# Optimization experiments

Hardware: AMD Instinct MI355X
Metric: run time of the kernel (lower is better)

Reference implementation:

```python
import jax, jax.numpy as jnp
import numpy as np

B, N, M, D_MODEL, D_K, D_V = 8, 2048, 2048, 1024, 1024, 1024
NEG = -1000000000.0


def setup_inputs() -> dict:
    key = jax.random.key(0)
    ks = jax.random.split(key, 10)
    s = 1.0 / np.sqrt(D_MODEL)
    return {
        "querys": jax.random.normal(ks[0], (B, N, D_MODEL), jnp.float32),
        "keys": jax.random.normal(ks[1], (B, M, D_MODEL), jnp.float32),
        "values": jax.random.normal(ks[2], (B, M, D_MODEL), jnp.float32),
        "mask": jax.random.randint(ks[3], (N, M), 0, 2, jnp.int32),
        "Wq": jax.random.normal(ks[4], (D_K, D_MODEL), jnp.float32) * s,
        "bq": jnp.zeros((D_K,), jnp.float32),
        "Wk": jax.random.normal(ks[5], (D_K, D_MODEL), jnp.float32) * s,
        "bk": jnp.zeros((D_K,), jnp.float32),
        "Wv": jax.random.normal(ks[6], (D_V, D_MODEL), jnp.float32) * s,
        "bv": jnp.zeros((D_V,), jnp.float32),
    }


def reference(querys, keys, values, mask, Wq, bq, Wk, bk, Wv, bv):
    # Linear projections (torch Linear: x @ W.T + b)
    q = querys @ Wq.T + bq          # [B, N, Dk]
    k = keys @ Wk.T + bk            # [B, M, Dk]
    v = values @ Wv.T + bv          # [B, M, Dv]
    # Original computes QK^T via broadcast mul+sum; GEMM form is identical math.
    # NOTE: no 1/sqrt(d) scaling, matching the source.
    scores = jnp.einsum('bnd,bmd->bnm', q, k)  # [B, N, M]
    scores = jnp.where(mask[None, :, :] == 0, NEG, scores)
    weights = jax.nn.softmax(scores, axis=2)
    out = jnp.einsum('bnm,bmd->bnd', weights, v)  # [B, N, Dv]
    return out
```

## Files before the change

kernel.cpp:

```cpp
#include <hip/hip_runtime.h>
#include <cstdint>

typedef __bf16 bf16_t;
typedef __bf16 bf16x8 __attribute__((ext_vector_type(8)));
typedef float f32x4 __attribute__((ext_vector_type(4)));

#define AS1 __attribute__((address_space(1)))
#define AS3 __attribute__((address_space(3)))

__device__ __forceinline__ void gload_lds16(const bf16_t* g, bf16_t* l) {
    __builtin_amdgcn_global_load_lds((const AS1 void*)g, (AS3 void*)l, 16, 0, 0);
}
__device__ __forceinline__ f32x4 mfma_bf16(bf16x8 a, bf16x8 b, f32x4 c) {
    return __builtin_amdgcn_mfma_f32_16x16x32_bf16(a, b, c, 0, 0, 0);
}

template <bool SPLIT, int BIAS, int OUTMODE>
__global__ __launch_bounds__(256) void gemm_bt(
    const bf16_t* __restrict__ Ah, const bf16_t* __restrict__ Al, long long strideA, int lda,
    const bf16_t* __restrict__ Bh, const bf16_t* __restrict__ Bl, long long strideB, int ldb,
    void* __restrict__ C0, void* __restrict__ C1, long long strideC, int ldc,
    const float* __restrict__ bias, int K)
{
    __shared__ bf16_t Ash[128 * 32];
    __shared__ bf16_t Bsh[128 * 32];
    __shared__ bf16_t Asl[SPLIT ? 128 * 32 : 8];
    __shared__ bf16_t Bsl[SPLIT ? 128 * 32 : 8];

    const int bz = blockIdx.z;
    const int rowBase = blockIdx.y * 128;
    const int colBase = blockIdx.x * 128;
    const bf16_t* AhB = Ah + (long long)bz * strideA;
    const bf16_t* BhB = Bh + (long long)bz * strideB;
    const bf16_t* AlB = SPLIT ? Al + (long long)bz * strideA : nullptr;
    const bf16_t* BlB = SPLIT ? Bl + (long long)bz * strideB : nullptr;

    const int t = threadIdx.x;
    const int lane = t & 63;
    const int w = t >> 6;
    const int wr = (w >> 1) * 64;
    const int wc = (w & 1) * 64;

    f32x4 acc[4][4] = {};

    const int r0 = t >> 2;
    const int kc0 = (((t & 3) ^ ((r0 >> 1) & 3)) * 8);

    for (int k0 = 0; k0 < K; k0 += 32) {
        const long long aoff0 = (long long)(rowBase + r0) * lda + k0 + kc0;
        const long long aoff1 = (long long)(rowBase + r0 + 64) * lda + k0 + kc0;
        const long long boff0 = (long long)(colBase + r0) * ldb + k0 + kc0;
        const long long boff1 = (long long)(colBase + r0 + 64) * ldb + k0 + kc0;
        gload_lds16(AhB + aoff0, &Ash[t * 8]);
        gload_lds16(AhB + aoff1, &Ash[(t + 256) * 8]);
        gload_lds16(BhB + boff0, &Bsh[t * 8]);
        gload_lds16(BhB + boff1, &Bsh[(t + 256) * 8]);
        if (SPLIT) {
            gload_lds16(AlB + aoff0, &Asl[t * 8]);
            gload_lds16(AlB + aoff1, &Asl[(t + 256) * 8]);
            gload_lds16(BlB + boff0, &Bsl[t * 8]);
            gload_lds16(BlB + boff1, &Bsl[(t + 256) * 8]);
        }
        __syncthreads();

        const int fr = lane & 15;
        const int kqs = (((lane >> 4) ^ ((lane >> 1) & 3)) * 8);
        bf16x8 ah[4], bh[4], al[4], bl[4];
#pragma unroll
        for (int mi = 0; mi < 4; mi++) {
            ah[mi] = *(const bf16x8*)&Ash[(wr + mi * 16 + fr) * 32 + kqs];
            if (SPLIT) al[mi] = *(const bf16x8*)&Asl[(wr + mi * 16 + fr) * 32 + kqs];
        }
#pragma unroll
        for (int ni = 0; ni < 4; ni++) {
            bh[ni] = *(const bf16x8*)&Bsh[(wc + ni * 16 + fr) * 32 + kqs];
            if (SPLIT) bl[ni] = *(const bf16x8*)&Bsl[(wc + ni * 16 + fr) * 32 + kqs];
        }

#pragma unroll
        for (int mi = 0; mi < 4; mi++)
#pragma unroll
            for (int ni = 0; ni < 4; ni++) {
                if (SPLIT) {
                    acc[mi][ni] = mfma_bf16(al[mi], bh[ni], acc[mi][ni]);
                    acc[mi][ni] = mfma_bf16(ah[mi], bl[ni], acc[mi][ni]);
                }
                acc[mi][ni] = mfma_bf16(ah[mi], bh[ni], acc[mi][ni]);
            }
        __syncthreads();
    }

    const int fc = lane & 15;
    const int fr4 = (lane >> 4) * 4;
#pragma unroll
    for (int mi = 0; mi < 4; mi++)
#pragma unroll
        for (int ni = 0; ni < 4; ni++)
#pragma unroll
            for (int rg = 0; rg < 4; rg++) {
                const int row = rowBase + wr + mi * 16 + fr4 + rg;
                const int col = colBase + wc + ni * 16 + fc;
                float v = acc[mi][ni][rg];
                if (BIAS == 1) v += bias[col];
                else if (BIAS == 2) v += bias[row];
                const long long off = (long long)bz * strideC + (long long)row * ldc + col;
                if (OUTMODE == 0) {
                    ((float*)C0)[off] = v;
                } else if (OUTMODE == 1) {
                    ((bf16_t*)C0)[off] = (bf16_t)v;
                } else {
                    const bf16_t h = (bf16_t)v;
                    ((bf16_t*)C0)[off] = h;
                    ((bf16_t*)C1)[off] = (bf16_t)(v - (float)h);
                }
            }
}

__global__ __launch_bounds__(256) void split_f32(const float* __restrict__ x,
                                                 bf16_t* __restrict__ h,
                                                 bf16_t* __restrict__ l)
{
    const long long i = ((long long)blockIdx.x * 256 + threadIdx.x) * 4;
    const float4 v = *(const float4*)&x[i];
    bf16_t hh[4], ll[4];
    const float vv[4] = {v.x, v.y, v.z, v.w};
#pragma unroll
    for (int j = 0; j < 4; j++) {
        hh[j] = (bf16_t)vv[j];
        ll[j] = (bf16_t)(vv[j] - (float)hh[j]);
    }
    *(short4*)&h[i] = *(short4*)hh;
    *(short4*)&l[i] = *(short4*)ll;
}

__global__ __launch_bounds__(256) void cast_f32(const float* __restrict__ x,
                                                bf16_t* __restrict__ y)
{
    const long long i = ((long long)blockIdx.x * 256 + threadIdx.x) * 4;
    const float4 v = *(const float4*)&x[i];
    bf16_t hh[4] = {(bf16_t)v.x, (bf16_t)v.y, (bf16_t)v.z, (bf16_t)v.w};
    *(short4*)&y[i] = *(short4*)hh;
}

__global__ __launch_bounds__(256) void softmax_rows(const float* __restrict__ S,
                                                    bf16_t* __restrict__ P,
                                                    const int* __restrict__ mask,
                                                    int n0)
{
    __shared__ float red[4];
    const long long r = blockIdx.x;
    const float* row = S + r * 2048;
    const int* mrow = mask + (long long)(n0 + (int)(r & 2047)) * 2048;
    const int t = threadIdx.x;

    float v[8];
#pragma unroll
    for (int i = 0; i < 8; i++) {
        const int j = i * 256 + t;
        v[i] = (mrow[j] != 0) ? row[j] : -1000000000.0f;
    }
    float m = v[0];
#pragma unroll
    for (int i = 1; i < 8; i++) m = fmaxf(m, v[i]);
#pragma unroll
    for (int off = 32; off; off >>= 1) m = fmaxf(m, __shfl_xor(m, off));
    if ((t & 63) == 0) red[t >> 6] = m;
    __syncthreads();
    const float rowmax = fmaxf(fmaxf(red[0], red[1]), fmaxf(red[2], red[3]));
    __syncthreads();

    float sum = 0.0f;
    float e[8];
#pragma unroll
    for (int i = 0; i < 8; i++) { e[i] = __expf(v[i] - rowmax); sum += e[i]; }
#pragma unroll
    for (int off = 32; off; off >>= 1) sum += __shfl_xor(sum, off);
    if ((t & 63) == 0) red[t >> 6] = sum;
    __syncthreads();
    const float inv = 1.0f / (red[0] + red[1] + red[2] + red[3]);

    bf16_t* prow = P + r * 2048;
#pragma unroll
    for (int i = 0; i < 8; i++) prow[i * 256 + t] = (bf16_t)(e[i] * inv);
}

extern "C" void kernel_launch(void* const* d_in, const int* in_sizes, int n_in,
                              void* d_out, int out_size, void* d_ws, size_t ws_size,
                              hipStream_t stream) {
    constexpr int Bb = 8, N = 2048, M = 2048, D = 1024;
    constexpr long long MB = 1LL << 20;

    const float* querys = (const float*)d_in[0];
    const float* keys   = (const float*)d_in[1];
    const float* values = (const float*)d_in[2];
    const int*   mask   = (const int*)d_in[3];
    const float* Wq = (const float*)d_in[4];
    const float* bq = (const float*)d_in[5];
    const float* Wk = (const float*)d_in[6];
    const float* bk = (const float*)d_in[7];
    const float* Wv = (const float*)d_in[8];
    const float* bv = (const float*)d_in[9];
    float* out = (float*)d_out;

    const long long w = (long long)ws_size;
    auto needB = [&](long long cb) { return 10 * MB + cb * 52 * MB; };
    int CB = 0;
    if      (w >= needB(8)) CB = 8;
    else if (w >= needB(4)) CB = 4;
    else if (w >= needB(2)) CB = 2;
    else if (w >= needB(1)) CB = 1;
    const bool batched = (CB != 0);
    int NCH = N;
    if (!batched) {
        CB = 1;
        NCH = (w >= 38 * MB + 512 * 2048 * 6) ? 512 : 128;
    }

    char* ws = (char*)d_ws;
    long long o = 0;
    auto carve = [&](long long bytes) { char* p = ws + o; o += bytes; return p; };
    bf16_t* WqH = (bf16_t*)carve(2 * MB);
    bf16_t* WqL = (bf16_t*)carve(2 * MB);
    bf16_t* WkH = (bf16_t*)carve(2 * MB);
    bf16_t* WkL = (bf16_t*)carve(2 * MB);
    bf16_t* WvB = (bf16_t*)carve(2 * MB);
    bf16_t* XH  = (bf16_t*)carve((long long)CB * 4 * MB);
    bf16_t* XL  = (bf16_t*)carve((long long)CB * 4 * MB);
    bf16_t* QH  = (bf16_t*)carve((long long)CB * 4 * MB);
    bf16_t* QL  = (bf16_t*)carve((long long)CB * 4 * MB);
    bf16_t* KH  = (bf16_t*)carve((long long)CB * 4 * MB);
    bf16_t* KL  = (bf16_t*)carve((long long)CB * 4 * MB);
    bf16_t* VT  = (bf16_t*)carve((long long)CB * 4 * MB);
    float*  S   = (float*)carve(batched ? (long long)CB * N * M * 4 : (long long)NCH * 2048 * 4);
    bf16_t* P   = (bf16_t*)carve(batched ? (long long)CB * N * M * 2 : (long long)NCH * 2048 * 2);

    dim3 blk(256);
    const long long grpElems = (long long)CB * N * D;

    split_f32<<<dim3((D * D) / 1024), blk, 0, stream>>>(Wq, WqH, WqL);
    split_f32<<<dim3((D * D) / 1024), blk, 0, stream>>>(Wk, WkH, WkL);
    cast_f32<<<dim3((D * D) / 1024), blk, 0, stream>>>(Wv, WvB);

    for (int b0 = 0; b0 < Bb; b0 += CB) {
        const long long xoff = (long long)b0 * N * D;
        split_f32<<<dim3(grpElems / 1024), blk, 0, stream>>>(querys + xoff, XH, XL);
        gemm_bt<true, 1, 2><<<dim3(D / 128, CB * N / 128, 1), blk, 0, stream>>>(
            XH, XL, 0, D, WqH, WqL, 0, D, QH, QL, 0, D, bq, D);
        split_f32<<<dim3(grpElems / 1024), blk, 0, stream>>>(keys + xoff, XH, XL);
        gemm_bt<true, 1, 2><<<dim3(D / 128, CB * M / 128, 1), blk, 0, stream>>>(
            XH, XL, 0, D, WkH, WkL, 0, D, KH, KL, 0, D, bk, D);
        cast_f32<<<dim3(grpElems / 1024), blk, 0, stream>>>(values + xoff, XH);
        gemm_bt<false, 2, 1><<<dim3(M / 128, D / 128, CB), blk, 0, stream>>>(
            WvB, nullptr, 0, D, XH, nullptr, (long long)M * D, D,
            VT, nullptr, (long long)D * M, M, bv, D);

        if (batched) {
            gemm_bt<true, 0, 0><<<dim3(M / 128, N / 128, CB), blk, 0, stream>>>(
                QH, QL, (long long)N * D, D,
                KH, KL, (long long)M * D, D,
                S, nullptr, (long long)N * M, M, nullptr, D);
            softmax_rows<<<dim3(CB * N), blk, 0, stream>>>(S, P, mask, 0);
            gemm_bt<false, 0, 0><<<dim3(D / 128, N / 128, CB), blk, 0, stream>>>(
                P, nullptr, (long long)N * M, M,
                VT, nullptr, (long long)D * M, M,
                out + xoff, nullptr, (long long)N * D, D, nullptr, M);
        } else {
            for (int z = 0; z < CB; z++) {
                for (int n0 = 0; n0 < N; n0 += NCH) {
                    gemm_bt<true, 0, 0><<<dim3(M / 128, NCH / 128, 1), blk, 0, stream>>>(
                        QH + ((long long)z * N + n0) * D, QL + ((long long)z * N + n0) * D, 0, D,
                        KH + (long long)z * M * D, KL + (long long)z * M * D, 0, D,
                        S, nullptr, 0, M, nullptr, D);
                    softmax_rows<<<dim3(NCH), blk, 0, stream>>>(S, P, mask, n0);
                    gemm_bt<false, 0, 0><<<dim3(D / 128, NCH / 128, 1), blk, 0, stream>>>(
                        P, nullptr, 0, M, VT + (long long)z * D * M, nullptr, 0, M,
                        out + ((long long)(b0 + z) * N + n0) * D, nullptr, 0, D, nullptr, M);
                }
            }
        }
    }
    (void)in_sizes; (void)n_in; (void)out_size;
}
```

Measured before the change: 962.8 us.

## Replace 128x128 GEMM with 256x256 four-stage pipelined 512-thread kernel

Replaces the 128x128-tile, 256-thread GEMM with a 256x256-tile, 8-wave kernel that uses a 4-deep LDS ring buffer fed by direct global-to-LDS loads. The split-bf16 terms are flattened into a single stream of K-stages, and each stage is split into two MFMA halves interleaved with prefetches, using explicit vmcnt waits, barriers and s_setprio. This aims to hide global memory latency and raise data reuse per block. In exchange it needs 128 KB of LDS per block and more registers, which lowers occupancy. The grid for the smaller GEMMs gets coarser, and the fallback chunk size is raised to 256 to match the new tile.

```diff
diff --git a/kernel.cpp b/kernel.cpp
--- a/kernel.cpp
+++ b/kernel.cpp
@@ -16,20 +16,17 @@
 }
 
 template <bool SPLIT, int BIAS, int OUTMODE>
-__global__ __launch_bounds__(256) void gemm_bt(
+__global__ __launch_bounds__(512, 2) void gemm256(
     const bf16_t* __restrict__ Ah, const bf16_t* __restrict__ Al, long long strideA, int lda,
     const bf16_t* __restrict__ Bh, const bf16_t* __restrict__ Bl, long long strideB, int ldb,
     void* __restrict__ C0, void* __restrict__ C1, long long strideC, int ldc,
     const float* __restrict__ bias, int K)
 {
-    __shared__ bf16_t Ash[128 * 32];
-    __shared__ bf16_t Bsh[128 * 32];
-    __shared__ bf16_t Asl[SPLIT ? 128 * 32 : 8];
-    __shared__ bf16_t Bsl[SPLIT ? 128 * 32 : 8];
+    __shared__ bf16_t lds[4 * 16384];
 
     const int bz = blockIdx.z;
-    const int rowBase = blockIdx.y * 128;
-    const int colBase = blockIdx.x * 128;
+    const int rowBase = blockIdx.y * 256;
+    const int colBase = blockIdx.x * 256;
     const bf16_t* AhB = Ah + (long long)bz * strideA;
     const bf16_t* BhB = Bh + (long long)bz * strideB;
     const bf16_t* AlB = SPLIT ? Al + (long long)bz * strideA : nullptr;
@@ -38,68 +35,113 @@
     const int t = threadIdx.x;
     const int lane = t & 63;
     const int w = t >> 6;
-    const int wr = (w >> 1) * 64;
-    const int wc = (w & 1) * 64;
-
-    f32x4 acc[4][4] = {};
+    const int wm = w >> 2;
+    const int wn = w & 3;
 
     const int r0 = t >> 2;
-    const int kc0 = (((t & 3) ^ ((r0 >> 1) & 3)) * 8);
-
-    for (int k0 = 0; k0 < K; k0 += 32) {
-        const long long aoff0 = (long long)(rowBase + r0) * lda + k0 + kc0;
-        const long long aoff1 = (long long)(rowBase + r0 + 64) * lda + k0 + kc0;
-        const long long boff0 = (long long)(colBase + r0) * ldb + k0 + kc0;
-        const long long boff1 = (long long)(colBase + r0 + 64) * ldb + k0 + kc0;
-        gload_lds16(AhB + aoff0, &Ash[t * 8]);
-        gload_lds16(AhB + aoff1, &Ash[(t + 256) * 8]);
-        gload_lds16(BhB + boff0, &Bsh[t * 8]);
-        gload_lds16(BhB + boff1, &Bsh[(t + 256) * 8]);
+    const int sl8 = ((t & 3) ^ ((r0 >> 1) & 3)) * 8;
+    const long long aoff0 = (long long)(rowBase + r0) * lda + sl8;
+    const long long aoff1 = (long long)(rowBase + r0 + 128) * lda + sl8;
+    const long long boff0 = (long long)(colBase + r0) * ldb + sl8;
+    const long long boff1 = (long long)(colBase + r0 + 128) * ldb + sl8;
+
+    const int NT = SPLIT ? (K >> 5) * 3 : (K >> 5);
+
+    auto tsrc = [&](int jt, const bf16_t*& sA, const bf16_t*& sB, long long& k0) {
         if (SPLIT) {
-            gload_lds16(AlB + aoff0, &Asl[t * 8]);
-            gload_lds16(AlB + aoff1, &Asl[(t + 256) * 8]);
-            gload_lds16(BlB + boff0, &Bsl[t * 8]);
-            gload_lds16(BlB + boff1, &Bsl[(t + 256) * 8]);
-        }
-        __syncthreads();
-
-        const int fr = lane & 15;
-        const int kqs = (((lane >> 4) ^ ((lane >> 1) & 3)) * 8);
-        bf16x8 ah[4], bh[4], al[4], bl[4];
-#pragma unroll
-        for (int mi = 0; mi < 4; mi++) {
-            ah[mi] = *(const bf16x8*)&Ash[(wr + mi * 16 + fr) * 32 + kqs];
-            if (SPLIT) al[mi] = *(const bf16x8*)&Asl[(wr + mi * 16 + fr) * 32 + kqs];
-        }
-#pragma unroll
-        for (int ni = 0; ni < 4; ni++) {
-            bh[ni] = *(const bf16x8*)&Bsh[(wc + ni * 16 + fr) * 32 + kqs];
-            if (SPLIT) bl[ni] = *(const bf16x8*)&Bsl[(wc + ni * 16 + fr) * 32 + kqs];
-        }
-
+            const int chunk = jt / 3;
+            const int term = jt - chunk * 3;
+            k0 = (long long)chunk * 32;
+            sA = (term == 2) ? AlB : AhB;
+            sB = (term == 1) ? BlB : BhB;
+        } else {
+            k0 = (long long)jt * 32;
+            sA = AhB; sB = BhB;
+        }
+    };
+
+    f32x4 acc[8][4] = {};
+
+    for (int jt = 0; jt < 3; ++jt) {
+        const bf16_t *sA, *sB; long long k0;
+        tsrc(jt, sA, sB, k0);
+        bf16_t* db = lds + jt * 16384;
+        gload_lds16(sA + aoff0 + k0, db + t * 8);
+        gload_lds16(sA + aoff1 + k0, db + 4096 + t * 8);
+        gload_lds16(sB + boff0 + k0, db + 8192 + t * 8);
+        gload_lds16(sB + boff1 + k0, db + 12288 + t * 8);
+    }
+    asm volatile("s_waitcnt vmcnt(8)" ::: "memory");
+    __builtin_amdgcn_s_barrier();
+
+    const int fr = lane & 15;
+    const int kqs = ((lane >> 4) ^ ((lane >> 1) & 3)) * 8;
+
+    for (int j = 0; j < NT; ++j) {
+        const bf16_t* bufA = lds + (j & 3) * 16384;
+        const bf16_t* bufB = bufA + 8192;
+        const int jt = j + 3;
+        const bool doStage = jt < NT;
+        const bf16_t *sA = nullptr, *sB = nullptr; long long k0 = 0;
+        if (doStage) tsrc(jt, sA, sB, k0);
+        bf16_t* db = lds + (jt & 3) * 16384;
+
+        bf16x8 a[4], b[4];
 #pragma unroll
         for (int mi = 0; mi < 4; mi++)
-#pragma unroll
-            for (int ni = 0; ni < 4; ni++) {
-                if (SPLIT) {
-                    acc[mi][ni] = mfma_bf16(al[mi], bh[ni], acc[mi][ni]);
-                    acc[mi][ni] = mfma_bf16(ah[mi], bl[ni], acc[mi][ni]);
-                }
-                acc[mi][ni] = mfma_bf16(ah[mi], bh[ni], acc[mi][ni]);
-            }
-        __syncthreads();
+            a[mi] = *(const bf16x8*)&bufA[(wm * 128 + mi * 16 + fr) * 32 + kqs];
+#pragma unroll
+        for (int ni = 0; ni < 4; ni++)
+            b[ni] = *(const bf16x8*)&bufB[(wn * 64 + ni * 16 + fr) * 32 + kqs];
+        if (doStage) {
+            gload_lds16(sA + aoff0 + k0, db + t * 8);
+            gload_lds16(sA + aoff1 + k0, db + 4096 + t * 8);
+        }
+        asm volatile("" ::: "memory");
+        __builtin_amdgcn_s_barrier();
+        __builtin_amdgcn_s_setprio(1);
+#pragma unroll
+        for (int mi = 0; mi < 4; mi++)
+#pragma unroll
+            for (int ni = 0; ni < 4; ni++)
+                acc[mi][ni] = mfma_bf16(a[mi], b[ni], acc[mi][ni]);
+        __builtin_amdgcn_s_setprio(0);
+        asm volatile("" ::: "memory");
+        __builtin_amdgcn_s_barrier();
+#pragma unroll
+        for (int mi = 0; mi < 4; mi++)
+            a[mi] = *(const bf16x8*)&bufA[(wm * 128 + (mi + 4) * 16 + fr) * 32 + kqs];
+        if (doStage) {
+            gload_lds16(sB + boff0 + k0, db + 8192 + t * 8);
+            gload_lds16(sB + boff1 + k0, db + 12288 + t * 8);
+        }
+        asm volatile("" ::: "memory");
+        __builtin_amdgcn_s_barrier();
+        __builtin_amdgcn_s_setprio(1);
+#pragma unroll
+        for (int mi = 0; mi < 4; mi++)
+#pragma unroll
+            for (int ni = 0; ni < 4; ni++)
+                acc[mi + 4][ni] = mfma_bf16(a[mi], b[ni], acc[mi + 4][ni]);
+        __builtin_amdgcn_s_setprio(0);
+        if (j + 1 < NT) {
+            if (j < NT - 3)       asm volatile("s_waitcnt vmcnt(8)" ::: "memory");
+            else if (j == NT - 3) asm volatile("s_waitcnt vmcnt(4)" ::: "memory");
+            else                  asm volatile("s_waitcnt vmcnt(0)" ::: "memory");
+            __builtin_amdgcn_s_barrier();
+        }
     }
 
     const int fc = lane & 15;
     const int fr4 = (lane >> 4) * 4;
 #pragma unroll
-    for (int mi = 0; mi < 4; mi++)
+    for (int mi = 0; mi < 8; mi++)
 #pragma unroll
         for (int ni = 0; ni < 4; ni++)
 #pragma unroll
             for (int rg = 0; rg < 4; rg++) {
-                const int row = rowBase + wr + mi * 16 + fr4 + rg;
-                const int col = colBase + wc + ni * 16 + fc;
+                const int row = rowBase + wm * 128 + mi * 16 + fr4 + rg;
+                const int col = colBase + wn * 64 + ni * 16 + fc;
                 float v = acc[mi][ni][rg];
                 if (BIAS == 1) v += bias[col];
                 else if (BIAS == 2) v += bias[row];
@@ -213,7 +255,7 @@
     int NCH = N;
     if (!batched) {
         CB = 1;
-        NCH = (w >= 38 * MB + 512 * 2048 * 6) ? 512 : 128;
+        NCH = (w >= 38 * MB + 512 * 2048 * 6) ? 512 : 256;
     }
 
     char* ws = (char*)d_ws;
@@ -234,7 +276,7 @@
     float*  S   = (float*)carve(batched ? (long long)CB * N * M * 4 : (long long)NCH * 2048 * 4);
     bf16_t* P   = (bf16_t*)carve(batched ? (long long)CB * N * M * 2 : (long long)NCH * 2048 * 2);
 
-    dim3 blk(256);
+    dim3 blk(256), blkG(512);
     const long long grpElems = (long long)CB * N * D;
 
     split_f32<<<dim3((D * D) / 1024), blk, 0, stream>>>(Wq, WqH, WqL);
@@ -244,35 +286,35 @@
     for (int b0 = 0; b0 < Bb; b0 += CB) {
         const long long xoff = (long long)b0 * N * D;
         split_f32<<<dim3(grpElems / 1024), blk, 0, stream>>>(querys + xoff, XH, XL);
-        gemm_bt<true, 1, 2><<<dim3(D / 128, CB * N / 128, 1), blk, 0, stream>>>(
+        gemm256<true, 1, 2><<<dim3(D / 256, CB * N / 256, 1), blkG, 0, stream>>>(
             XH, XL, 0, D, WqH, WqL, 0, D, QH, QL, 0, D, bq, D);
         split_f32<<<dim3(grpElems / 1024), blk, 0, stream>>>(keys + xoff, XH, XL);
-        gemm_bt<true, 1, 2><<<dim3(D / 128, CB * M / 128, 1), blk, 0, stream>>>(
+        gemm256<true, 1, 2><<<dim3(D / 256, CB * M / 256, 1), blkG, 0, stream>>>(
             XH, XL, 0, D, WkH, WkL, 0, D, KH, KL, 0, D, bk, D);
         cast_f32<<<dim3(grpElems / 1024), blk, 0, stream>>>(values + xoff, XH);
-        gemm_bt<false, 2, 1><<<dim3(M / 128, D / 128, CB), blk, 0, stream>>>(
+        gemm256<false, 2, 1><<<dim3(M / 256, D / 256, CB), blkG, 0, stream>>>(
             WvB, nullptr, 0, D, XH, nullptr, (long long)M * D, D,
             VT, nullptr, (long long)D * M, M, bv, D);
 
         if (batched) {
-            gemm_bt<true, 0, 0><<<dim3(M / 128, N / 128, CB), blk, 0, stream>>>(
+            gemm256<true, 0, 0><<<dim3(M / 256, N / 256, CB), blkG, 0, stream>>>(
                 QH, QL, (long long)N * D, D,
                 KH, KL, (long long)M * D, D,
                 S, nullptr, (long long)N * M, M, nullptr, D);
             softmax_rows<<<dim3(CB * N), blk, 0, stream>>>(S, P, mask, 0);
-            gemm_bt<false, 0, 0><<<dim3(D / 128, N / 128, CB), blk, 0, stream>>>(
+            gemm256<false, 0, 0><<<dim3(D / 256, N / 256, CB), blkG, 0, stream>>>(
                 P, nullptr, (long long)N * M, M,
                 VT, nullptr, (long long)D * M, M,
                 out + xoff, nullptr, (long long)N * D, D, nullptr, M);
         } else {
             for (int z = 0; z < CB; z++) {
                 for (int n0 = 0; n0 < N; n0 += NCH) {
-                    gemm_bt<true, 0, 0><<<dim3(M / 128, NCH / 128, 1), blk, 0, stream>>>(
+                    gemm256<true, 0, 0><<<dim3(M / 256, NCH / 256, 1), blkG, 0, stream>>>(
                         QH + ((long long)z * N + n0) * D, QL + ((long long)z * N + n0) * D, 0, D,
                         KH + (long long)z * M * D, KL + (long long)z * M * D, 0, D,
                         S, nullptr, 0, M, nullptr, D);
                     softmax_rows<<<dim3(NCH), blk, 0, stream>>>(S, P, mask, n0);
-                    gemm_bt<false, 0, 0><<<dim3(D / 128, NCH / 128, 1), blk, 0, stream>>>(
+                    gemm256<false, 0, 0><<<dim3(D / 256, NCH / 256, 1), blkG, 0, stream>>>(
                         P, nullptr, 0, M, VT + (long long)z * D * M, nullptr, 0, M,
                         out + ((long long)(b0 + z) * N + n0) * D, nullptr, 0, D, nullptr, M);
                 }
```

After: 1.069 ms. 11.0% more time.
